# Performance work log

Measured on AMD Instinct MI355X. Metric: run time of the kernel, lower is better.

Reference implementation:

```python
import jax, jax.numpy as jnp
import numpy as np

B, D, S, E = 256, 5, 30, 768
H1, H2, FF, OUT = 512, 512, 256, 2


def setup_inputs() -> dict:
    key = jax.random.key(0)
    ks = iter(jax.random.split(key, 40))

    def p(shape, scale=0.05):
        return jax.random.normal(next(ks), shape, jnp.float32) * scale

    return {
        "sentence_feats": jax.random.normal(next(ks), (B, D, S, E), jnp.float32),
        "time_feats": jax.random.uniform(next(ks), (B, D, S), jnp.float32),
        "len_tweets": jax.random.randint(next(ks), (B, D), 1, S + 1, jnp.int32),
        # TimeLSTM (lstm1)
        "Wd_w": p((H1, H1)), "Wd_b": p((H1,)),
        "Wall_w": p((4 * H1, H1)), "Wall_b": p((4 * H1,)),
        "Uall_w": p((4 * H1, E)), "Uall_b": p((4 * H1,)),
        # attn1
        "A1_W1_w": p((H1, H1)), "A1_W1_b": p((H1,)),
        "A1_W2_w": p((H1, H1)), "A1_W2_b": p((H1,)),
        "A1_V_w": p((1, H1)), "A1_V_b": p((1,)),
        # nn.LSTM (lstm2), gate order i,f,g,o
        "L2_Wih": p((4 * H2, H1)), "L2_Whh": p((4 * H2, H2)),
        "L2_bih": p((4 * H2,)), "L2_bhh": p((4 * H2,)),
        # attn2
        "A2_W1_w": p((H2, H2)), "A2_W1_b": p((H2,)),
        "A2_W2_w": p((H2, H2)), "A2_W2_b": p((H2,)),
        "A2_V_w": p((1, H2)), "A2_V_b": p((1,)),
        # head
        "lin3_w": p((FF, H2)), "lin3_b": p((FF,)),
        "lin4_w": p((OUT, FF)), "lin4_b": p((OUT,)),
    }


def _time_lstm(x, t, Wd_w, Wd_b, Wall_w, Wall_b, Uall_w, Uall_b):
    # x: (N,S,E), t: (N,S) -> o-gate outputs (N,S,H) (the torch module stacks `o`, not `h`)
    N = x.shape[0]
    H = Wd_w.shape[0]
    ux = jnp.einsum('nse,ge->nsg', x, Uall_w) + Uall_b  # (N,S,4H), hoisted out of recurrence

    def step(carry, inp):
        h, c = carry
        ux_s, t_s = inp
        c_s1 = jnp.tanh(c @ Wd_w.T + Wd_b)
        c_adj = c - c_s1 + c_s1 * t_s[:, None]
        gates = jax.nn.sigmoid(h @ Wall_w.T + Wall_b + ux_s)
        f, i, o, c_tmp = jnp.split(gates, 4, axis=1)  # all sigmoid, incl. c_tmp (as in source)
        c = f * c_adj + i * c_tmp
        h = o * jnp.tanh(c)
        return (h, c), o

    init = (jnp.zeros((N, H), x.dtype), jnp.zeros((N, H), x.dtype))
    _, os = jax.lax.scan(step, init, (ux.transpose(1, 0, 2), t.T))
    return os.transpose(1, 0, 2)  # (N,S,H)


def _std_lstm(x, Wih, Whh, bih, bhh):
    # PyTorch nn.LSTM, 1 layer, batch_first. x: (B,T,I) -> (hs (B,T,H), h_n (B,H))
    Bn = x.shape[0]
    H = Whh.shape[1]
    xi = jnp.einsum('bti,gi->btg', x, Wih) + bih + bhh  # (B,T,4H)

    def step(carry, xi_t):
        h, c = carry
        g = xi_t + h @ Whh.T
        i, f, gg, o = jnp.split(g, 4, axis=1)
        c = jax.nn.sigmoid(f) * c + jax.nn.sigmoid(i) * jnp.tanh(gg)
        h = jax.nn.sigmoid(o) * jnp.tanh(c)
        return (h, c), h

    init = (jnp.zeros((Bn, H), x.dtype), jnp.zeros((Bn, H), x.dtype))
    (h_n, _), hs = jax.lax.scan(step, init, xi.transpose(1, 0, 2))
    return hs.transpose(1, 0, 2), h_n


def _forward(sentence_feats, time_feats, Wd_w, Wd_b, Wall_w, Wall_b, Uall_w, Uall_b,
             A1_W1_w, A1_W1_b, A1_W2_w, A1_W2_b, A1_V_w, A1_V_b,
             L2_Wih, L2_Whh, L2_bih, L2_bhh,
             A2_W1_w, A2_W1_b, A2_W2_w, A2_W2_b, A2_V_w, A2_V_b,
             lin3_w, lin3_b, lin4_w, lin4_b, len_tweets):
    x = sentence_feats.transpose(1, 0, 2, 3)  # (D,B,S,E)
    t = time_feats.transpose(1, 0, 2)         # (D,B,S)
    lens = len_tweets.transpose(1, 0)          # (D,B)
    d, b, s, e = x.shape

    # run TimeLSTM over all days at once (days are independent, shared zero init)
    outs = _time_lstm(x.reshape(d * b, s, e), t.reshape(d * b, s),
                      Wd_w, Wd_b, Wall_w, Wall_b, Uall_w, Uall_b).reshape(d, b, s, H1)

    # Faithful to the source's inner loop: temp_hn ends up as the LAST batch
    # element's output at index len-1, shared across the whole batch of that day.
    idx = lens[:, -1] - 1  # (D,)
    last = jnp.take_along_axis(outs[:, -1], idx[:, None, None], axis=1)[:, 0]  # (D,H1)

    # attn1: score = V(tanh(W1(last) + W2(full))), mask by lens, softmax over S
    s1 = jnp.tanh((last @ A1_W1_w.T + A1_W1_b)[:, None, None, :]
                  + jnp.einsum('dbsh,gh->dbsg', outs, A1_W2_w) + A1_W2_b)
    score = jnp.einsum('dbsh,oh->dbso', s1, A1_V_w) + A1_V_b  # (D,B,S,1)
    mask = jnp.arange(s)[None, None, :] < lens[:, :, None]     # (D,B,S)
    score = jnp.where(mask[..., None], score, -jnp.inf)
    aw = jax.nn.softmax(score, axis=2)
    lstm1_out = jnp.sum(aw * outs, axis=2).transpose(1, 0, 2)  # (B,D,H1)

    lstm2_out, hn2 = _std_lstm(lstm1_out, L2_Wih, L2_Whh, L2_bih, L2_bhh)  # (B,D,H2),(B,H2)

    # attn2 over days
    s2 = jnp.tanh((hn2 @ A2_W1_w.T + A2_W1_b)[:, None, :]
                  + lstm2_out @ A2_W2_w.T + A2_W2_b)
    score2 = s2 @ A2_V_w.T + A2_V_b                 # (B,D,1)
    aw2 = jax.nn.softmax(score2, axis=1)
    ctx = jnp.sum(aw2 * lstm2_out, axis=1)          # (B,H2)

    h3 = jax.nn.relu(ctx @ lin3_w.T + lin3_b)       # dropout = identity (eval mode)
    return h3 @ lin4_w.T + lin4_b                   # (B,OUT)


def reference(sentence_feats, time_feats, len_tweets, Wd_w, Wd_b, Wall_w, Wall_b, Uall_w, Uall_b,
              A1_W1_w, A1_W1_b, A1_W2_w, A1_W2_b, A1_V_w, A1_V_b,
              L2_Wih, L2_Whh, L2_bih, L2_bhh,
              A2_W1_w, A2_W1_b, A2_W2_w, A2_W2_b, A2_V_w, A2_V_b,
              lin3_w, lin3_b, lin4_w, lin4_b):
    return _forward(sentence_feats, time_feats, Wd_w, Wd_b, Wall_w, Wall_b, Uall_w, Uall_b,
                    A1_W1_w, A1_W1_b, A1_W2_w, A1_W2_b, A1_V_w, A1_V_b,
                    L2_Wih, L2_Whh, L2_bih, L2_bhh,
                    A2_W1_w, A2_W1_b, A2_W2_w, A2_W2_b, A2_V_w, A2_V_b,
                    lin3_w, lin3_b, lin4_w, lin4_b, len_tweets)
```

## Files before the change

kernel.cpp:

```cpp
#include <hip/hip_runtime.h>
#include <math.h>

typedef _Float16 f16;
typedef _Float16 f16x4 __attribute__((ext_vector_type(4)));
typedef _Float16 f16x8 __attribute__((ext_vector_type(8)));
typedef float f32x4 __attribute__((ext_vector_type(4)));

#define DEV static __device__ __forceinline__

#define OFF_X16    ((size_t)0)
#define OFF_UX     ((size_t)58982400)
#define OFF_OUTS   ((size_t)216268800)
#define OFF_WD     ((size_t)255590400)
#define OFF_WALLP  ((size_t)256114688)
#define OFF_UP     ((size_t)258211840)
#define OFF_W2     ((size_t)261357568)
#define OFF_WIHP   ((size_t)261881856)
#define OFF_WHHP   ((size_t)263979008)
#define OFF_A2W1C  ((size_t)266076160)
#define OFF_A2W2C  ((size_t)266600448)
#define OFF_L3WC   ((size_t)267124736)
#define OFF_BALLP  ((size_t)267386880)
#define OFF_BIHP   ((size_t)267395072)
#define OFF_H16    ((size_t)267403264)
#define OFF_C16    ((size_t)270024704)
#define OFF_C32    ((size_t)272646144)
#define WS_NEED    ((size_t)277889024)
#define OFF_SCORE  ((size_t)0)
#define OFF_W1L    ((size_t)153600)
#define OFF_L1O32  ((size_t)163840)
#define OFF_L1O16  ((size_t)2785280)
#define OFF_XI2    ((size_t)4096000)
#define OFF_C2     ((size_t)14581760)
#define OFF_H2     ((size_t)15630336)
#define OFF_L2O32  ((size_t)16154624)
#define OFF_L2O16  ((size_t)18776064)
#define OFF_U2     ((size_t)20086784)
#define OFF_V2     ((size_t)22708224)
#define OFF_CTX16  ((size_t)23232512)
#define OFF_H3     ((size_t)23494656)
#define OFF_TFT    ((size_t)23756800)

DEV float sigf(float x) { return 1.f / (1.f + __expf(-x)); }
DEV float tanhfast(float x) { float e = __expf(2.f * x); return 1.f - 2.f / (e + 1.f); }
DEV int permrow(int c) { return (((c >> 4) & 3) << 9) | ((c >> 6) << 4) | (c & 15); }

DEV void gload16(const f16* g, f16x8* lds) {
  __builtin_amdgcn_global_load_lds((const __attribute__((address_space(1))) void*)g,
                                   (__attribute__((address_space(3))) void*)lds, 16, 0, 0);
}

DEV void gemm_core(const f16* __restrict__ A, const f16* __restrict__ Bt, int K,
                   int rowBase, int colBase, f16x8* sh, f32x4 (&acc)[4][4]) {
  const int t = threadIdx.x, lane = t & 63, w = t >> 6;
  const int wr = (w >> 1) * 64, wc = (w & 1) * 64;
  const f16* Arow = A + (size_t)rowBase * K;
  const f16* Brow = Bt + (size_t)colBase * K;
  auto stage = [&](f16x8* dstBase, const f16* src, int k0) {
#pragma unroll
    for (int i = 0; i < 4; ++i) {
      int c = i * 256 + t; int r = c >> 3; int cc = (c & 7) ^ (r & 7);
      gload16(src + (size_t)r * K + (k0 + cc * 8), dstBase + i * 256 + (t & 192));
    }
  };
  stage(sh, Arow, 0);
  stage(sh + 2048, Brow, 0);
  const int nk = K >> 6;
  for (int kt = 0; kt < nk; ++kt) {
    const int cur = kt & 1;
    if (kt + 1 < nk) {
      stage(sh + (cur ^ 1) * 1024, Arow, (kt + 1) * 64);
      stage(sh + 2048 + (cur ^ 1) * 1024, Brow, (kt + 1) * 64);
      asm volatile("s_waitcnt vmcnt(8)" ::: "memory");
    } else {
      asm volatile("s_waitcnt vmcnt(0)" ::: "memory");
    }
    __builtin_amdgcn_s_barrier();
    __builtin_amdgcn_sched_barrier(0);
    const f16x8* shA = sh + cur * 1024;
    const f16x8* shB = sh + 2048 + cur * 1024;
    const int rr = lane & 15, chb = lane >> 4;
#pragma unroll
    for (int kk = 0; kk < 2; ++kk) {
      const int ch = kk * 4 + chb;
      f16x8 af[4], bf[4];
#pragma unroll
      for (int m = 0; m < 4; ++m) { int row = wr + m * 16 + rr; af[m] = shA[row * 8 + (ch ^ (row & 7))]; }
#pragma unroll
      for (int n = 0; n < 4; ++n) { int row = wc + n * 16 + rr; bf[n] = shB[row * 8 + (ch ^ (row & 7))]; }
#pragma unroll
      for (int m = 0; m < 4; ++m)
#pragma unroll
        for (int n = 0; n < 4; ++n)
          acc[m][n] = __builtin_amdgcn_mfma_f32_16x16x32_f16(af[m], bf[n], acc[m][n], 0, 0, 0);
    }
    __builtin_amdgcn_sched_barrier(0);
    __builtin_amdgcn_s_barrier();
  }
}

template <int ACT, bool O32, bool O16>
__global__ __launch_bounds__(256, 2) void k_gemm(const f16* __restrict__ A, const f16* __restrict__ Bt,
                                                 int K, int N, const float* __restrict__ bias,
                                                 float* __restrict__ C32, f16* __restrict__ C16) {
  __shared__ f16x8 sh[4096];
  const int rb = blockIdx.y * 128, cb = blockIdx.x * 128;
  f32x4 acc[4][4] = {};
  gemm_core(A, Bt, K, rb, cb, sh, acc);
  const int t = threadIdx.x, lane = t & 63, w = t >> 6;
  const int wr = (w >> 1) * 64, wc = (w & 1) * 64, ec = lane & 15, er = (lane >> 4) * 4;
#pragma unroll
  for (int m = 0; m < 4; ++m)
#pragma unroll
    for (int n = 0; n < 4; ++n) {
      const int c = cb + wc + n * 16 + ec;
      const float bv = bias ? bias[c] : 0.f;
#pragma unroll
      for (int j = 0; j < 4; ++j) {
        const int r = rb + wr + m * 16 + er + j;
        float v = acc[m][n][j] + bv;
        if (ACT == 3) v = fmaxf(v, 0.f);
        if (O32) C32[(size_t)r * N + c] = v;
        if (O16) C16[(size_t)r * N + c] = (f16)v;
      }
    }
}

__global__ __launch_bounds__(256, 1) void k_stepf(
    const f16* __restrict__ hin, const f16* __restrict__ cin16, const float* __restrict__ cin32,
    const f16* __restrict__ Wallp, const f16* __restrict__ Wd16,
    const f16* __restrict__ ux, const float* __restrict__ ballp, const float* __restrict__ Wd_b,
    const float* __restrict__ tft,
    float* __restrict__ cout32, f16* __restrict__ cout16, f16* __restrict__ hout,
    f16* __restrict__ outs, int s) {
  __shared__ f16x8 shA[2048];
  __shared__ f16x8 shB[2048];
  __shared__ f16x8 shC[2048];
  __shared__ f16x8 shD[512];
  __shared__ f16x8 shU[2048];
  __shared__ f16x8 shE[1024];
  const int t = threadIdx.x, lane = t & 63, w = t >> 6;
  const int rb = ((int)blockIdx.x >> 4) * 128;
  const int cg = (int)blockIdx.x & 15;
  const int wr = (w >> 1) * 64, wc = (w & 1) * 64;
  const int rr = lane & 15, chb = lane >> 4;
  const int ec = lane & 15, er = (lane >> 4) * 4;
  const int h = cg * 32 + (w & 1) * 16 + ec;
  const int hcol = (w & 1) * 16 + ec;
  const f16* Ah = hin + (size_t)rb * 512;
  const f16* Ac = cin16 + (size_t)rb * 512;
  const f16* Bw = Wallp + (size_t)cg * 128 * 512;
  const f16* Bd = Wd16 + (size_t)cg * 32 * 512;
  float bW[4];
#pragma unroll
  for (int n = 0; n < 4; ++n) bW[n] = ballp[cg * 128 + wc + n * 16 + ec];
  const float bD = Wd_b[h];
  const f16* shUf = (const f16*)shU;
  const float* shEf = (const float*)shE;
  const int kbase = (wc >> 3) + (ec >> 3);
  f32x4 acc[4][4] = {};
  f32x4 acc2[4] = {};

  auto stage128 = [&](f16x8* dstBase, const f16* src, int k0) {
#pragma unroll
    for (int i = 0; i < 4; ++i) {
      int c = i * 256 + t; int r = c >> 3; int cc = (c & 7) ^ (r & 7);
      gload16(src + (size_t)r * 512 + (k0 + cc * 8), dstBase + i * 256 + (t & 192));
    }
  };
  auto stage32 = [&](f16x8* dstBase, const f16* src, int k0) {
    const int r = t >> 3; const int cc = (t & 7) ^ (r & 7);
    gload16(src + (size_t)r * 512 + (k0 + cc * 8), dstBase + (t & 192));
  };
  auto stageU = [&]() {
#pragma unroll
    for (int i = 0; i < 8; ++i) {
      int c = i * 256 + t; int lr = c >> 4; int k = c & 15;
      int klog = k ^ (((lr >> 2) & 3) << 1);
      gload16(ux + ((size_t)(rb + lr) * 30 + s) * 2048 + cg * 128 + klog * 8,
              shU + i * 256 + (t & 192));
    }
  };
  auto stageE = [&]() {
#pragma unroll
    for (int i = 0; i < 4; ++i) {
      int c = i * 256 + t; int lr = c >> 3; int k = c & 7;
      int klog = k ^ (((lr >> 2) & 1) << 2);
      gload16((const f16*)(cin32 + (size_t)(rb + lr) * 512 + cg * 32 + klog * 4),
              shE + i * 256 + (t & 192));
    }
  };

  if (s == 0) {
    stageU();
    stageE();
    asm volatile("s_waitcnt vmcnt(0)" ::: "memory");
    __builtin_amdgcn_s_barrier();
  } else {
    stage128(shA, Ah, 0);
    stage128(shB, Bw, 0);
    stage128(shC, Ac, 0);
    stage32(shD, Bd, 0);
    stageU();
    stageE();
    for (int kt = 0; kt < 8; ++kt) {
      const int cur = kt & 1;
      if (kt < 7) {
        stage128(shA + (cur ^ 1) * 1024, Ah, (kt + 1) * 64);
        stage128(shB + (cur ^ 1) * 1024, Bw, (kt + 1) * 64);
        stage128(shC + (cur ^ 1) * 1024, Ac, (kt + 1) * 64);
        stage32(shD + (cur ^ 1) * 256, Bd, (kt + 1) * 64);
        asm volatile("s_waitcnt vmcnt(13)" ::: "memory");
      } else {
        asm volatile("s_waitcnt vmcnt(0)" ::: "memory");
      }
      __builtin_amdgcn_s_barrier();
      __builtin_amdgcn_sched_barrier(0);
      const f16x8* pA = shA + cur * 1024;
      const f16x8* pB = shB + cur * 1024;
      const f16x8* pC = shC + cur * 1024;
      const f16x8* pD = shD + cur * 256;
#pragma unroll
      for (int kk = 0; kk < 2; ++kk) {
        const int ch = kk * 4 + chb;
        f16x8 af[4], bf[4], cf[4], df;
#pragma unroll
        for (int m = 0; m < 4; ++m) {
          const int row = wr + m * 16 + rr;
          af[m] = pA[row * 8 + (ch ^ (row & 7))];
          cf[m] = pC[row * 8 + (ch ^ (row & 7))];
        }
#pragma unroll
        for (int n = 0; n < 4; ++n) { const int row = wc + n * 16 + rr; bf[n] = pB[row * 8 + (ch ^ (row & 7))]; }
        { const int row = (w & 1) * 16 + rr; df = pD[row * 8 + (ch ^ (row & 7))]; }
#pragma unroll
        for (int m = 0; m < 4; ++m) {
#pragma unroll
          for (int n = 0; n < 4; ++n)
            acc[m][n] = __builtin_amdgcn_mfma_f32_16x16x32_f16(af[m], bf[n], acc[m][n], 0, 0, 0);
          acc2[m] = __builtin_amdgcn_mfma_f32_16x16x32_f16(cf[m], df, acc2[m], 0, 0, 0);
        }
      }
      __builtin_amdgcn_sched_barrier(0);
      __builtin_amdgcn_s_barrier();
    }
  }

#pragma unroll
  for (int m = 0; m < 4; ++m)
#pragma unroll
    for (int j = 0; j < 4; ++j) {
      const int lr = wr + m * 16 + er + j;
      const int r = rb + lr;
      const float tv = tft[s * 1280 + r];
      const int sU = ((lr >> 2) & 3) << 1;
      const float u0 = (float)shUf[(lr * 16 + ((kbase + 0) ^ sU)) * 8 + (ec & 7)];
      const float u1 = (float)shUf[(lr * 16 + ((kbase + 2) ^ sU)) * 8 + (ec & 7)];
      const float u2v = (float)shUf[(lr * 16 + ((kbase + 4) ^ sU)) * 8 + (ec & 7)];
      const float u3 = (float)shUf[(lr * 16 + ((kbase + 6) ^ sU)) * 8 + (ec & 7)];
      const float p0 = acc[m][0][j] + bW[0] + u0;
      const float p1 = acc[m][1][j] + bW[1] + u1;
      const float p2 = acc[m][2][j] + bW[2] + u2v;
      const float p3 = acc[m][3][j] + bW[3] + u3;
      const float f = sigf(p0), i = sigf(p1), o = sigf(p2), ct = sigf(p3);
      const float cs = tanhfast(acc2[m][j] + bD);
      const int sE = ((lr >> 2) & 1) << 2;
      const float c_old = shEf[(lr * 8 + ((hcol >> 2) ^ sE)) * 4 + (hcol & 3)];
      const float cadj = c_old - cs + cs * tv;
      const float cn = f * cadj + i * ct;
      cout32[(size_t)r * 512 + h] = cn;
      cout16[(size_t)r * 512 + h] = (f16)cn;
      hout[(size_t)r * 512 + h] = (f16)(o * tanhfast(cn));
      outs[((size_t)r * 30 + s) * 512 + h] = (f16)o;
    }
}

__global__ __launch_bounds__(256, 2) void k_l2step(const f16* __restrict__ hin, const f16* __restrict__ Whhp,
    const float* __restrict__ xi2, const float* __restrict__ cin, float* __restrict__ cout,
    f16* __restrict__ hout, float* __restrict__ l2o32, f16* __restrict__ l2o16, int ts) {
  __shared__ f16x8 sh[4096];
  const int rb = (blockIdx.x >> 4) * 128, cg = blockIdx.x & 15;
  f32x4 acc[4][4] = {};
  gemm_core(hin, Whhp, 512, rb, cg * 128, sh, acc);
  const int t = threadIdx.x, lane = t & 63, w = t >> 6;
  const int wr = (w >> 1) * 64, wc = (w & 1) * 64, ec = lane & 15, er = (lane >> 4) * 4;
  const int h = cg * 32 + (w & 1) * 16 + ec;
#pragma unroll
  for (int m = 0; m < 4; ++m)
#pragma unroll
    for (int j = 0; j < 4; ++j) {
      const int r = rb + wr + m * 16 + er + j;
      const size_t xb = ((size_t)r * 5 + ts) * 2048 + cg * 128 + wc + ec;
      const float p0 = acc[m][0][j] + xi2[xb];
      const float p1 = acc[m][1][j] + xi2[xb + 16];
      const float p2 = acc[m][2][j] + xi2[xb + 32];
      const float p3 = acc[m][3][j] + xi2[xb + 48];
      const float ii = sigf(p0), ff = sigf(p1), gg = tanhfast(p2), oo = sigf(p3);
      const float cn = ff * cin[(size_t)r * 512 + h] + ii * gg;
      const float hn = oo * tanhfast(cn);
      cout[(size_t)r * 512 + h] = cn;
      hout[(size_t)r * 512 + h] = (f16)hn;
      const size_t ob = ((size_t)r * 5 + ts) * 512 + h;
      l2o32[ob] = hn;
      l2o16[ob] = (f16)hn;
    }
}

__global__ __launch_bounds__(256, 2) void k_score(const f16* __restrict__ outs, const f16* __restrict__ W2t,
    const float* __restrict__ W2b, const float* __restrict__ w1l, const float* __restrict__ V,
    float* __restrict__ score) {
  __shared__ f16x8 sh[4096];
  const int rb = blockIdx.y * 128, cb = blockIdx.x * 128;
  f32x4 acc[4][4] = {};
  gemm_core(outs, W2t, 512, rb, cb, sh, acc);
  const int t = threadIdx.x, lane = t & 63, w = t >> 6;
  const int wr = (w >> 1) * 64, wc = (w & 1) * 64, ec = lane & 15, er = (lane >> 4) * 4;
  float* sacc = (float*)sh;
  if (t < 128) sacc[t] = 0.f;
  __syncthreads();
#pragma unroll
  for (int m = 0; m < 4; ++m)
#pragma unroll
    for (int j = 0; j < 4; ++j) {
      const int lr = wr + m * 16 + er + j;
      const int r = rb + lr;
      const int d = (r / 30) >> 8;
      float p = 0.f;
#pragma unroll
      for (int n = 0; n < 4; ++n) {
        const int c = cb + wc + n * 16 + ec;
        p += V[c] * tanhfast(acc[m][n][j] + W2b[c] + w1l[d * 512 + c]);
      }
      p += __shfl_xor(p, 1); p += __shfl_xor(p, 2); p += __shfl_xor(p, 4); p += __shfl_xor(p, 8);
      if (ec == 0) atomicAdd(&sacc[lr], p);
    }
  __syncthreads();
  if (t < 128) atomicAdd(&score[rb + t], sacc[t]);
}

__global__ __launch_bounds__(256) void k_w1last(const f16* __restrict__ outs, const int* __restrict__ lens,
                                                const float* __restrict__ W1, const float* __restrict__ W1b,
                                                float* __restrict__ w1l) {
  __shared__ float lastv[512];
  const int d = blockIdx.x;
  const int idx = lens[255 * 5 + d] - 1;
  const size_t row = ((size_t)(d * 256 + 255) * 30 + idx) * 512;
  for (int h = threadIdx.x; h < 512; h += 256) lastv[h] = (float)outs[row + h];
  __syncthreads();
  for (int h = threadIdx.x; h < 512; h += 256) {
    const float* wr = W1 + (size_t)h * 512;
    float p = W1b[h];
    for (int k = 0; k < 512; ++k) p += lastv[k] * wr[k];
    w1l[d * 512 + h] = p;
  }
}

__global__ __launch_bounds__(256) void k_attn1(const float* __restrict__ score, const f16* __restrict__ outs,
                                               const int* __restrict__ lens,
                                               float* __restrict__ l1o32, f16* __restrict__ l1o16) {
  __shared__ float saw[32];
  const int n = blockIdx.x;
  const int d = n >> 8, b = n & 255;
  const int len = lens[b * 5 + d];
  const int t = threadIdx.x, lane = t & 63, w = t >> 6;
  if (w == 0) {
    const bool valid = lane < len;
    float sc = valid ? score[(size_t)n * 30 + lane] : -INFINITY;
    float mx = sc;
#pragma unroll
    for (int off = 32; off > 0; off >>= 1) mx = fmaxf(mx, __shfl_xor(mx, off));
    float e = valid ? __expf(sc - mx) : 0.f;
    float sm = e;
#pragma unroll
    for (int off = 32; off > 0; off >>= 1) sm += __shfl_xor(sm, off);
    if (lane < 30) saw[lane] = e / sm;
  }
  __syncthreads();
  for (int h = t; h < 512; h += 256) {
    float acc = 0.f;
    for (int s = 0; s < len; ++s) acc += saw[s] * (float)outs[((size_t)n * 30 + s) * 512 + h];
    const size_t o = ((size_t)b * 5 + d) * 512 + h;
    l1o32[o] = acc;
    l1o16[o] = (f16)acc;
  }
}

__global__ __launch_bounds__(256, 2) void k_uv(const f16* __restrict__ l2o16, const f16* __restrict__ A2W2c,
    const f16* __restrict__ h2fin, const f16* __restrict__ A2W1c,
    const float* __restrict__ bu, const float* __restrict__ bv,
    float* __restrict__ u2, float* __restrict__ v2) {
  __shared__ f16x8 sh[4096];
  const int bid = blockIdx.x;
  const f16* A; const f16* B; const float* bias; float* out; int rb, cb;
  if (bid < 40) { A = l2o16; B = A2W2c; bias = bu; out = u2; rb = (bid >> 2) * 128; cb = (bid & 3) * 128; }
  else { int b2 = bid - 40; A = h2fin; B = A2W1c; bias = bv; out = v2; rb = (b2 >> 2) * 128; cb = (b2 & 3) * 128; }
  f32x4 acc[4][4] = {};
  gemm_core(A, B, 512, rb, cb, sh, acc);
  const int t = threadIdx.x, lane = t & 63, w = t >> 6;
  const int wr = (w >> 1) * 64, wc = (w & 1) * 64, ec = lane & 15, er = (lane >> 4) * 4;
#pragma unroll
  for (int m = 0; m < 4; ++m)
#pragma unroll
    for (int n = 0; n < 4; ++n) {
      const int c = cb + wc + n * 16 + ec;
      const float bvv = bias[c];
#pragma unroll
      for (int j = 0; j < 4; ++j) out[(size_t)(rb + wr + m * 16 + er + j) * 512 + c] = acc[m][n][j] + bvv;
    }
}

__global__ __launch_bounds__(256) void k_attn2(const float* __restrict__ u2, const float* __restrict__ v2,
                                               const float* __restrict__ l2o, const float* __restrict__ V2,
                                               const float* __restrict__ V2b, f16* __restrict__ ctx16) {
  __shared__ float ssc[8];
  __shared__ float saw[8];
  const int b = blockIdx.x;
  const int t = threadIdx.x, lane = t & 63, w = t >> 6;
  for (int tt = w; tt < 5; tt += 4) {
    const float* ur = u2 + ((size_t)b * 5 + tt) * 512;
    const float* vr = v2 + (size_t)b * 512;
    float p = 0.f;
#pragma unroll
    for (int j = 0; j < 8; ++j) { int h = lane * 8 + j; p += V2[h] * tanhfast(ur[h] + vr[h]); }
#pragma unroll
    for (int off = 32; off > 0; off >>= 1) p += __shfl_down(p, off);
    if (lane == 0) ssc[tt] = p + V2b[0];
  }
  __syncthreads();
  if (w == 0) {
    const bool valid = lane < 5;
    float sc = valid ? ssc[lane] : -INFINITY;
    float mx = sc;
#pragma unroll
    for (int off = 32; off > 0; off >>= 1) mx = fmaxf(mx, __shfl_xor(mx, off));
    float e = valid ? __expf(sc - mx) : 0.f;
    float sm = e;
#pragma unroll
    for (int off = 32; off > 0; off >>= 1) sm += __shfl_xor(sm, off);
    if (valid) saw[lane] = e / sm;
  }
  __syncthreads();
  for (int h = t; h < 512; h += 256) {
    float a = 0.f;
#pragma unroll
    for (int tt = 0; tt < 5; ++tt) a += saw[tt] * l2o[((size_t)b * 5 + tt) * 512 + h];
    ctx16[(size_t)b * 512 + h] = (f16)a;
  }
}

__global__ __launch_bounds__(256) void k_final(const float* __restrict__ h3, const float* __restrict__ W4,
                                               const float* __restrict__ b4, float* __restrict__ out) {
  const int idx = blockIdx.x * 256 + threadIdx.x;
  const int b = idx >> 1, o = idx & 1;
  const float* hr = h3 + b * 256;
  const float* wr = W4 + o * 256;
  float p = b4[o];
  for (int j = 0; j < 256; ++j) p += hr[j] * wr[j];
  out[idx] = p;
}

__global__ __launch_bounds__(256) void k_castx(const float* __restrict__ sf, f16* __restrict__ x16) {
  const int total = 7372800;
  for (int e = blockIdx.x * 256 + threadIdx.x; e < total; e += gridDim.x * 256) {
    const int row = e / 192, k = e - row * 192;
    const int b = row / 150, rem = row - b * 150;
    const int d = rem / 30, s = rem - d * 30;
    const int orow = (d * 256 + b) * 30 + s;
    const float4 v = ((const float4*)sf)[e];
    f16x4 o = {(f16)v.x, (f16)v.y, (f16)v.z, (f16)v.w};
    ((f16x4*)x16)[(size_t)orow * 192 + k] = o;
  }
}

struct CastArgs { const float* src[5]; f16* dst[5]; int cnt4[5]; };
__global__ __launch_bounds__(256) void k_castw(CastArgs a) {
  int g = blockIdx.x * 256 + threadIdx.x;
#pragma unroll
  for (int si = 0; si < 5; ++si) {
    if (g < a.cnt4[si]) {
      const float4 v = ((const float4*)a.src[si])[g];
      f16x4 o = {(f16)v.x, (f16)v.y, (f16)v.z, (f16)v.w};
      ((f16x4*)a.dst[si])[g] = o;
      return;
    }
    g -= a.cnt4[si];
  }
}

struct PermArgs { const float* src[4]; f16* dst[4]; int k4[4]; int cnt4[4]; };
__global__ __launch_bounds__(256) void k_castperm(PermArgs a) {
  int g = blockIdx.x * 256 + threadIdx.x;
#pragma unroll
  for (int si = 0; si < 4; ++si) {
    if (g < a.cnt4[si]) {
      const int K4 = a.k4[si];
      const int c = g / K4, k = g - c * K4;
      const float4 v = ((const float4*)a.src[si])[(size_t)permrow(c) * K4 + k];
      f16x4 o = {(f16)v.x, (f16)v.y, (f16)v.z, (f16)v.w};
      ((f16x4*)a.dst[si])[(size_t)c * K4 + k] = o;
      return;
    }
    g -= a.cnt4[si];
  }
}

__global__ __launch_bounds__(256) void k_zero(f16* h16a, f16* c16a, float* c32a,
    float* ballp, float* bihp, const float* Wall_b, const float* Uall_b,
    const float* bih, const float* bhh, float* tft, const float* tf) {
  const int i = blockIdx.x * 256 + threadIdx.x;
  if (i < 655360) { h16a[i] = (f16)0.f; c16a[i] = (f16)0.f; c32a[i] = 0.f; }
  if (i < 2048) {
    const int p = permrow(i);
    ballp[i] = Wall_b[p] + Uall_b[p];
    bihp[i] = bih[p] + bhh[p];
  }
  if (i < 38400) {
    const int s = i / 1280, r = i - s * 1280;
    const int d = r >> 8, b = r & 255;
    tft[i] = tf[((size_t)b * 5 + d) * 30 + s];
  }
}

__global__ __launch_bounds__(256) void k_scoreinit(float* score, const float* Vb, f16* h2a, float* c2a) {
  const int i = blockIdx.x * 256 + threadIdx.x;
  if (i < 38400) score[i] = Vb[0];
  if (i < 131072) { h2a[i] = (f16)0.f; c2a[i] = 0.f; }
}

extern "C" void kernel_launch(void* const* d_in, const int* in_sizes, int n_in,
                              void* d_out, int out_size, void* d_ws, size_t ws_size,
                              hipStream_t stream) {
  const float* sf     = (const float*)d_in[0];
  const float* tf     = (const float*)d_in[1];
  const int*   lens   = (const int*)d_in[2];
  const float* Wd_w   = (const float*)d_in[3];
  const float* Wd_b   = (const float*)d_in[4];
  const float* Wall_w = (const float*)d_in[5];
  const float* Wall_b = (const float*)d_in[6];
  const float* Uall_w = (const float*)d_in[7];
  const float* Uall_b = (const float*)d_in[8];
  const float* A1W1   = (const float*)d_in[9];
  const float* A1W1b  = (const float*)d_in[10];
  const float* A1W2   = (const float*)d_in[11];
  const float* A1W2b  = (const float*)d_in[12];
  const float* A1V    = (const float*)d_in[13];
  const float* A1Vb   = (const float*)d_in[14];
  const float* Wih    = (const float*)d_in[15];
  const float* Whh    = (const float*)d_in[16];
  const float* bih    = (const float*)d_in[17];
  const float* bhh    = (const float*)d_in[18];
  const float* A2W1   = (const float*)d_in[19];
  const float* A2W1b  = (const float*)d_in[20];
  const float* A2W2   = (const float*)d_in[21];
  const float* A2W2b  = (const float*)d_in[22];
  const float* A2V    = (const float*)d_in[23];
  const float* A2Vb   = (const float*)d_in[24];
  const float* L3w    = (const float*)d_in[25];
  const float* L3b    = (const float*)d_in[26];
  const float* L4w    = (const float*)d_in[27];
  const float* L4b    = (const float*)d_in[28];

  if (ws_size < WS_NEED) return;
  char* ws = (char*)d_ws;
  f16*   x16    = (f16*)(ws + OFF_X16);
  f16*   ux16   = (f16*)(ws + OFF_UX);
  f16*   outs16 = (f16*)(ws + OFF_OUTS);
  f16*   Wd16   = (f16*)(ws + OFF_WD);
  f16*   Wallp  = (f16*)(ws + OFF_WALLP);
  f16*   U16p   = (f16*)(ws + OFF_UP);
  f16*   W216   = (f16*)(ws + OFF_W2);
  f16*   Wihp   = (f16*)(ws + OFF_WIHP);
  f16*   Whhp   = (f16*)(ws + OFF_WHHP);
  f16*   A2W116 = (f16*)(ws + OFF_A2W1C);
  f16*   A2W216 = (f16*)(ws + OFF_A2W2C);
  f16*   L316   = (f16*)(ws + OFF_L3WC);
  float* ballp  = (float*)(ws + OFF_BALLP);
  float* bihp   = (float*)(ws + OFF_BIHP);
  f16*   h16b[2]  = {(f16*)(ws + OFF_H16), (f16*)(ws + OFF_H16 + 1310720)};
  f16*   c16b[2]  = {(f16*)(ws + OFF_C16), (f16*)(ws + OFF_C16 + 1310720)};
  float* c32b[2]  = {(float*)(ws + OFF_C32), (float*)(ws + OFF_C32 + 2621440)};
  float* score  = (float*)(ws + OFF_SCORE);
  float* w1l    = (float*)(ws + OFF_W1L);
  float* l1o32  = (float*)(ws + OFF_L1O32);
  f16*   l1o16  = (f16*)(ws + OFF_L1O16);
  float* xi2    = (float*)(ws + OFF_XI2);
  float* c2b[2] = {(float*)(ws + OFF_C2), (float*)(ws + OFF_C2 + 524288)};
  f16*   h2b[2] = {(f16*)(ws + OFF_H2), (f16*)(ws + OFF_H2 + 262144)};
  float* l2o32  = (float*)(ws + OFF_L2O32);
  f16*   l2o16  = (f16*)(ws + OFF_L2O16);
  float* u2     = (float*)(ws + OFF_U2);
  float* v2     = (float*)(ws + OFF_V2);
  f16*   ctx16  = (f16*)(ws + OFF_CTX16);
  float* h3     = (float*)(ws + OFF_H3);
  float* tft    = (float*)(ws + OFF_TFT);

  k_castx<<<2048, 256, 0, stream>>>(sf, x16);
  CastArgs ca;
  ca.src[0] = Wd_w;  ca.dst[0] = Wd16;   ca.cnt4[0] = 65536;
  ca.src[1] = A1W2;  ca.dst[1] = W216;   ca.cnt4[1] = 65536;
  ca.src[2] = A2W1;  ca.dst[2] = A2W116; ca.cnt4[2] = 65536;
  ca.src[3] = A2W2;  ca.dst[3] = A2W216; ca.cnt4[3] = 65536;
  ca.src[4] = L3w;   ca.dst[4] = L316;   ca.cnt4[4] = 32768;
  k_castw<<<1152, 256, 0, stream>>>(ca);
  PermArgs pa;
  pa.src[0] = Wall_w; pa.dst[0] = Wallp; pa.k4[0] = 128; pa.cnt4[0] = 262144;
  pa.src[1] = Uall_w; pa.dst[1] = U16p;  pa.k4[1] = 192; pa.cnt4[1] = 393216;
  pa.src[2] = Wih;    pa.dst[2] = Wihp;  pa.k4[2] = 128; pa.cnt4[2] = 262144;
  pa.src[3] = Whh;    pa.dst[3] = Whhp;  pa.k4[3] = 128; pa.cnt4[3] = 262144;
  k_castperm<<<4608, 256, 0, stream>>>(pa);

  k_gemm<0, false, true><<<dim3(16, 300), 256, 0, stream>>>(x16, U16p, 768, 2048, nullptr, nullptr, ux16);

  k_zero<<<2560, 256, 0, stream>>>(h16b[0], c16b[0], c32b[0], ballp, bihp, Wall_b, Uall_b, bih, bhh,
                                   tft, tf);

  for (int s = 0; s < 30; ++s) {
    const int pi = s & 1, po = pi ^ 1;
    k_stepf<<<160, 256, 0, stream>>>(h16b[pi], c16b[pi], c32b[pi], Wallp, Wd16, ux16, ballp, Wd_b, tft,
                                     c32b[po], c16b[po], h16b[po], outs16, s);
  }

  k_w1last<<<5, 256, 0, stream>>>(outs16, lens, A1W1, A1W1b, w1l);
  k_scoreinit<<<512, 256, 0, stream>>>(score, A1Vb, h2b[0], c2b[0]);
  k_score<<<dim3(4, 300), 256, 0, stream>>>(outs16, W216, A1W2b, w1l, A1V, score);
  k_attn1<<<1280, 256, 0, stream>>>(score, outs16, lens, l1o32, l1o16);

  k_gemm<0, true, false><<<dim3(16, 10), 256, 0, stream>>>(l1o16, Wihp, 512, 2048, bihp, xi2, nullptr);
  for (int ts = 0; ts < 5; ++ts) {
    const int pi = ts & 1, po = pi ^ 1;
    k_l2step<<<32, 256, 0, stream>>>(h2b[pi], Whhp, xi2, c2b[pi], c2b[po], h2b[po], l2o32, l2o16, ts);
  }

  k_uv<<<48, 256, 0, stream>>>(l2o16, A2W216, h2b[1], A2W116, A2W2b, A2W1b, u2, v2);
  k_attn2<<<256, 256, 0, stream>>>(u2, v2, l2o32, A2V, A2Vb, ctx16);

  k_gemm<3, true, false><<<dim3(2, 2), 256, 0, stream>>>(ctx16, L316, 512, 256, L3b, h3, nullptr);
  k_final<<<2, 256, 0, stream>>>(h3, L4w, L4b, (float*)d_out);
}
```

Baseline: 1.003 ms.

## Use 256x256 double-buffered GEMM tiles for Ux and attn1 score; merge small launches

Adds a 512-thread GEMM core with 256x256 output tiles and double-buffered LDS staging that overlaps the next k-slice's global loads with MFMA work. It is used for the big x·Uall projection and the attention-1 score GEMM. Larger tiles raise operand reuse and halve the number of blocks. The weight cast and permute kernels are merged into one launch, and score/LSTM2 initialisation moves into k_zero, removing two launches. The cost is one block per CU and a bigger accumulator register footprint, which may cut latency hiding and risk register spills.

```diff
diff --git a/kernel.cpp b/kernel.cpp
--- a/kernel.cpp
+++ b/kernel.cpp
@@ -99,6 +99,114 @@
   }
 }
 
+DEV void gemm_core256(const f16* __restrict__ A, const f16* __restrict__ Bt, int K,
+                      int rowBase, int colBase, f16x8 (&shA)[2][2048], f16x8 (&shB)[2][2048],
+                      f32x4 (&acc)[8][4]) {
+  const int t = threadIdx.x, lane = t & 63, w = t >> 6;
+  const int wm = w >> 2, wn = w & 3;
+  const f16* Arow = A + (size_t)rowBase * K;
+  const f16* Brow = Bt + (size_t)colBase * K;
+  auto stage = [&](f16x8* dst, const f16* src, int k0) {
+#pragma unroll
+    for (int i = 0; i < 4; ++i) {
+      int c = i * 512 + t; int r = c >> 3; int cc = (c & 7) ^ (r & 7);
+      gload16(src + (size_t)r * K + (k0 + cc * 8), dst + i * 512 + (t & 448));
+    }
+  };
+  stage(shA[0], Arow, 0);
+  stage(shB[0], Brow, 0);
+  const int nk = K >> 6;
+  for (int kt = 0; kt < nk; ++kt) {
+    const int cur = kt & 1;
+    if (kt + 1 < nk) {
+      stage(shA[cur ^ 1], Arow, (kt + 1) * 64);
+      stage(shB[cur ^ 1], Brow, (kt + 1) * 64);
+      asm volatile("s_waitcnt vmcnt(8)" ::: "memory");
+    } else {
+      asm volatile("s_waitcnt vmcnt(0)" ::: "memory");
+    }
+    __builtin_amdgcn_s_barrier();
+    __builtin_amdgcn_sched_barrier(0);
+    const f16x8* pA = shA[cur];
+    const f16x8* pB = shB[cur];
+    const int rr = lane & 15, chb = lane >> 4;
+#pragma unroll
+    for (int kk = 0; kk < 2; ++kk) {
+      const int ch = kk * 4 + chb;
+      f16x8 bf[4];
+#pragma unroll
+      for (int n = 0; n < 4; ++n) { int row = wn * 64 + n * 16 + rr; bf[n] = pB[row * 8 + (ch ^ (row & 7))]; }
+#pragma unroll
+      for (int m = 0; m < 8; ++m) {
+        int row = wm * 128 + m * 16 + rr;
+        f16x8 af = pA[row * 8 + (ch ^ (row & 7))];
+#pragma unroll
+        for (int n = 0; n < 4; ++n)
+          acc[m][n] = __builtin_amdgcn_mfma_f32_16x16x32_f16(af, bf[n], acc[m][n], 0, 0, 0);
+      }
+    }
+    __builtin_amdgcn_sched_barrier(0);
+    __builtin_amdgcn_s_barrier();
+  }
+}
+
+__global__ __launch_bounds__(512, 1) void k_gemm256(const f16* __restrict__ A, const f16* __restrict__ Bt,
+                                                    int K, int N, f16* __restrict__ C16) {
+  __shared__ f16x8 shA[2][2048];
+  __shared__ f16x8 shB[2][2048];
+  const int rb = blockIdx.y * 256, cb = blockIdx.x * 256;
+  f32x4 acc[8][4] = {};
+  gemm_core256(A, Bt, K, rb, cb, shA, shB, acc);
+  const int t = threadIdx.x, lane = t & 63, w = t >> 6;
+  const int wm = w >> 2, wn = w & 3;
+  const int ec = lane & 15, er = (lane >> 4) * 4;
+#pragma unroll
+  for (int m = 0; m < 8; ++m)
+#pragma unroll
+    for (int n = 0; n < 4; ++n) {
+      const int c = cb + wn * 64 + n * 16 + ec;
+#pragma unroll
+      for (int j = 0; j < 4; ++j) {
+        const int r = rb + wm * 128 + m * 16 + er + j;
+        C16[(size_t)r * N + c] = (f16)acc[m][n][j];
+      }
+    }
+}
+
+__global__ __launch_bounds__(512, 1) void k_score2(const f16* __restrict__ outs, const f16* __restrict__ W2t,
+    const float* __restrict__ W2b, const float* __restrict__ w1l, const float* __restrict__ V,
+    float* __restrict__ score) {
+  __shared__ f16x8 shA[2][2048];
+  __shared__ f16x8 shB[2][2048];
+  __shared__ float sacc[256];
+  const int rb = blockIdx.y * 256, cb = blockIdx.x * 256;
+  f32x4 acc[8][4] = {};
+  gemm_core256(outs, W2t, 512, rb, cb, shA, shB, acc);
+  const int t = threadIdx.x, lane = t & 63, w = t >> 6;
+  const int wm = w >> 2, wn = w & 3;
+  const int ec = lane & 15, er = (lane >> 4) * 4;
+  if (t < 256) sacc[t] = 0.f;
+  __syncthreads();
+#pragma unroll
+  for (int m = 0; m < 8; ++m)
+#pragma unroll
+    for (int j = 0; j < 4; ++j) {
+      const int lr = wm * 128 + m * 16 + er + j;
+      const int r = rb + lr;
+      const int d = (r / 30) >> 8;
+      float p = 0.f;
+#pragma unroll
+      for (int n = 0; n < 4; ++n) {
+        const int c = cb + wn * 64 + n * 16 + ec;
+        p += V[c] * tanhfast(acc[m][n][j] + W2b[c] + w1l[d * 512 + c]);
+      }
+      p += __shfl_xor(p, 1); p += __shfl_xor(p, 2); p += __shfl_xor(p, 4); p += __shfl_xor(p, 8);
+      if (ec == 0) atomicAdd(&sacc[lr], p);
+    }
+  __syncthreads();
+  if (t < 256) atomicAdd(&score[rb + t], sacc[t]);
+}
+
 template <int ACT, bool O32, bool O16>
 __global__ __launch_bounds__(256, 2) void k_gemm(const f16* __restrict__ A, const f16* __restrict__ Bt,
                                                  int K, int N, const float* __restrict__ bias,
@@ -306,38 +414,6 @@
     }
 }
 
-__global__ __launch_bounds__(256, 2) void k_score(const f16* __restrict__ outs, const f16* __restrict__ W2t,
-    const float* __restrict__ W2b, const float* __restrict__ w1l, const float* __restrict__ V,
-    float* __restrict__ score) {
-  __shared__ f16x8 sh[4096];
-  const int rb = blockIdx.y * 128, cb = blockIdx.x * 128;
-  f32x4 acc[4][4] = {};
-  gemm_core(outs, W2t, 512, rb, cb, sh, acc);
-  const int t = threadIdx.x, lane = t & 63, w = t >> 6;
-  const int wr = (w >> 1) * 64, wc = (w & 1) * 64, ec = lane & 15, er = (lane >> 4) * 4;
-  float* sacc = (float*)sh;
-  if (t < 128) sacc[t] = 0.f;
-  __syncthreads();
-#pragma unroll
-  for (int m = 0; m < 4; ++m)
-#pragma unroll
-    for (int j = 0; j < 4; ++j) {
-      const int lr = wr + m * 16 + er + j;
-      const int r = rb + lr;
-      const int d = (r / 30) >> 8;
-      float p = 0.f;
-#pragma unroll
-      for (int n = 0; n < 4; ++n) {
-        const int c = cb + wc + n * 16 + ec;
-        p += V[c] * tanhfast(acc[m][n][j] + W2b[c] + w1l[d * 512 + c]);
-      }
-      p += __shfl_xor(p, 1); p += __shfl_xor(p, 2); p += __shfl_xor(p, 4); p += __shfl_xor(p, 8);
-      if (ec == 0) atomicAdd(&sacc[lr], p);
-    }
-  __syncthreads();
-  if (t < 128) atomicAdd(&score[rb + t], sacc[t]);
-}
-
 __global__ __launch_bounds__(256) void k_w1last(const f16* __restrict__ outs, const int* __restrict__ lens,
                                                 const float* __restrict__ W1, const float* __restrict__ W1b,
                                                 float* __restrict__ w1l) {
@@ -472,30 +548,16 @@
   }
 }
 
-struct CastArgs { const float* src[5]; f16* dst[5]; int cnt4[5]; };
-__global__ __launch_bounds__(256) void k_castw(CastArgs a) {
+struct WPArgs { const float* src[9]; f16* dst[9]; int k4[9]; int cnt4[9]; int perm[9]; };
+__global__ __launch_bounds__(256) void k_castwp(WPArgs a) {
   int g = blockIdx.x * 256 + threadIdx.x;
 #pragma unroll
-  for (int si = 0; si < 5; ++si) {
-    if (g < a.cnt4[si]) {
-      const float4 v = ((const float4*)a.src[si])[g];
-      f16x4 o = {(f16)v.x, (f16)v.y, (f16)v.z, (f16)v.w};
-      ((f16x4*)a.dst[si])[g] = o;
-      return;
-    }
-    g -= a.cnt4[si];
-  }
-}
-
-struct PermArgs { const float* src[4]; f16* dst[4]; int k4[4]; int cnt4[4]; };
-__global__ __launch_bounds__(256) void k_castperm(PermArgs a) {
-  int g = blockIdx.x * 256 + threadIdx.x;
-#pragma unroll
-  for (int si = 0; si < 4; ++si) {
+  for (int si = 0; si < 9; ++si) {
     if (g < a.cnt4[si]) {
       const int K4 = a.k4[si];
       const int c = g / K4, k = g - c * K4;
-      const float4 v = ((const float4*)a.src[si])[(size_t)permrow(c) * K4 + k];
+      const int srow = a.perm[si] ? permrow(c) : c;
+      const float4 v = ((const float4*)a.src[si])[(size_t)srow * K4 + k];
       f16x4 o = {(f16)v.x, (f16)v.y, (f16)v.z, (f16)v.w};
       ((f16x4*)a.dst[si])[(size_t)c * K4 + k] = o;
       return;
@@ -506,7 +568,8 @@
 
 __global__ __launch_bounds__(256) void k_zero(f16* h16a, f16* c16a, float* c32a,
     float* ballp, float* bihp, const float* Wall_b, const float* Uall_b,
-    const float* bih, const float* bhh, float* tft, const float* tf) {
+    const float* bih, const float* bhh, float* tft, const float* tf,
+    float* score, const float* Vb, f16* h2a, float* c2a) {
   const int i = blockIdx.x * 256 + threadIdx.x;
   if (i < 655360) { h16a[i] = (f16)0.f; c16a[i] = (f16)0.f; c32a[i] = 0.f; }
   if (i < 2048) {
@@ -518,12 +581,8 @@
     const int s = i / 1280, r = i - s * 1280;
     const int d = r >> 8, b = r & 255;
     tft[i] = tf[((size_t)b * 5 + d) * 30 + s];
-  }
-}
-
-__global__ __launch_bounds__(256) void k_scoreinit(float* score, const float* Vb, f16* h2a, float* c2a) {
-  const int i = blockIdx.x * 256 + threadIdx.x;
-  if (i < 38400) score[i] = Vb[0];
+    score[i] = Vb[0];
+  }
   if (i < 131072) { h2a[i] = (f16)0.f; c2a[i] = 0.f; }
 }
 
@@ -595,24 +654,22 @@
   float* tft    = (float*)(ws + OFF_TFT);
 
   k_castx<<<2048, 256, 0, stream>>>(sf, x16);
-  CastArgs ca;
-  ca.src[0] = Wd_w;  ca.dst[0] = Wd16;   ca.cnt4[0] = 65536;
-  ca.src[1] = A1W2;  ca.dst[1] = W216;   ca.cnt4[1] = 65536;
-  ca.src[2] = A2W1;  ca.dst[2] = A2W116; ca.cnt4[2] = 65536;
-  ca.src[3] = A2W2;  ca.dst[3] = A2W216; ca.cnt4[3] = 65536;
-  ca.src[4] = L3w;   ca.dst[4] = L316;   ca.cnt4[4] = 32768;
-  k_castw<<<1152, 256, 0, stream>>>(ca);
-  PermArgs pa;
-  pa.src[0] = Wall_w; pa.dst[0] = Wallp; pa.k4[0] = 128; pa.cnt4[0] = 262144;
-  pa.src[1] = Uall_w; pa.dst[1] = U16p;  pa.k4[1] = 192; pa.cnt4[1] = 393216;
-  pa.src[2] = Wih;    pa.dst[2] = Wihp;  pa.k4[2] = 128; pa.cnt4[2] = 262144;
-  pa.src[3] = Whh;    pa.dst[3] = Whhp;  pa.k4[3] = 128; pa.cnt4[3] = 262144;
-  k_castperm<<<4608, 256, 0, stream>>>(pa);
-
-  k_gemm<0, false, true><<<dim3(16, 300), 256, 0, stream>>>(x16, U16p, 768, 2048, nullptr, nullptr, ux16);
+  WPArgs wa;
+  wa.src[0] = Wd_w;   wa.dst[0] = Wd16;   wa.k4[0] = 128; wa.cnt4[0] = 65536;  wa.perm[0] = 0;
+  wa.src[1] = A1W2;   wa.dst[1] = W216;   wa.k4[1] = 128; wa.cnt4[1] = 65536;  wa.perm[1] = 0;
+  wa.src[2] = A2W1;   wa.dst[2] = A2W116; wa.k4[2] = 128; wa.cnt4[2] = 65536;  wa.perm[2] = 0;
+  wa.src[3] = A2W2;   wa.dst[3] = A2W216; wa.k4[3] = 128; wa.cnt4[3] = 65536;  wa.perm[3] = 0;
+  wa.src[4] = L3w;    wa.dst[4] = L316;   wa.k4[4] = 128; wa.cnt4[4] = 32768;  wa.perm[4] = 0;
+  wa.src[5] = Wall_w; wa.dst[5] = Wallp;  wa.k4[5] = 128; wa.cnt4[5] = 262144; wa.perm[5] = 1;
+  wa.src[6] = Uall_w; wa.dst[6] = U16p;   wa.k4[6] = 192; wa.cnt4[6] = 393216; wa.perm[6] = 1;
+  wa.src[7] = Wih;    wa.dst[7] = Wihp;   wa.k4[7] = 128; wa.cnt4[7] = 262144; wa.perm[7] = 1;
+  wa.src[8] = Whh;    wa.dst[8] = Whhp;   wa.k4[8] = 128; wa.cnt4[8] = 262144; wa.perm[8] = 1;
+  k_castwp<<<5760, 256, 0, stream>>>(wa);
+
+  k_gemm256<<<dim3(8, 150), 512, 0, stream>>>(x16, U16p, 768, 2048, ux16);
 
   k_zero<<<2560, 256, 0, stream>>>(h16b[0], c16b[0], c32b[0], ballp, bihp, Wall_b, Uall_b, bih, bhh,
-                                   tft, tf);
+                                   tft, tf, score, A1Vb, h2b[0], c2b[0]);
 
   for (int s = 0; s < 30; ++s) {
     const int pi = s & 1, po = pi ^ 1;
@@ -621,8 +678,7 @@
   }
 
   k_w1last<<<5, 256, 0, stream>>>(outs16, lens, A1W1, A1W1b, w1l);
-  k_scoreinit<<<512, 256, 0, stream>>>(score, A1Vb, h2b[0], c2b[0]);
-  k_score<<<dim3(4, 300), 256, 0, stream>>>(outs16, W216, A1W2b, w1l, A1V, score);
+  k_score2<<<dim3(2, 150), 512, 0, stream>>>(outs16, W216, A1W2b, w1l, A1V, score);
   k_attn1<<<1280, 256, 0, stream>>>(score, outs16, lens, l1o32, l1o16);
 
   k_gemm<0, true, false><<<dim3(16, 10), 256, 0, stream>>>(l1o16, Wihp, 512, 2048, bihp, xi2, nullptr);
```

Result: no change. 1.016 ms (+1.2%).
